# Optimization experiments

Measured on AMD Instinct MI355X. Metric: run time of the kernel, lower is better.

## Reference

```python
import jax, jax.numpy as jnp
import numpy as np

N = 100000
NNZ = 1600000
DIM = 128
IN_FEAT = 128


def spmm(vals, rows, cols, x, n):
    # sparse [n,n] COO @ dense [n,d] -> [n,d]
    return jax.ops.segment_sum(vals[:, None] * x[cols], rows, num_segments=n)


def setup_inputs() -> dict:
    key = jax.random.key(0)
    ks = jax.random.split(key, 7)
    inputs = jax.random.normal(ks[0], (N, IN_FEAT), dtype=jnp.float32)
    # TruncatedNormal(stddev=1/sqrt(fan_in)) approximated by scaled normal
    w1 = jax.random.normal(ks[1], (N, DIM), dtype=jnp.float32) / np.sqrt(N)
    w2 = jax.random.normal(ks[2], (IN_FEAT, DIM), dtype=jnp.float32) / np.sqrt(IN_FEAT)
    wg = jax.random.normal(ks[3], (DIM, 1), dtype=jnp.float32)  # glorot-ish, dim=1 gate
    A_vals = jax.random.uniform(ks[4], (NNZ,), dtype=jnp.float32)
    A_rows = jax.random.randint(ks[5], (NNZ,), 0, N, dtype=jnp.int32)
    A_cols = jax.random.randint(ks[6], (NNZ,), 0, N, dtype=jnp.int32)
    return {"inputs": inputs, "w1": w1, "w2": w2, "wg": wg,
            "A_vals": A_vals, "A_rows": A_rows, "A_cols": A_cols}


def reference(inputs, w1, w2, wg, A_vals, A_rows, A_cols):
    n = w1.shape[0]
    # aw layer: relu(A @ w1)
    a = jax.nn.relu(spmm(A_vals, A_rows, A_cols, w1, n))          # [N, dim]
    # axw layer: relu(A @ (X @ w2))
    b = jax.nn.relu(spmm(A_vals, A_rows, A_cols, inputs @ w2, n))  # [N, dim]
    # highway gate: T = sigmoid(b @ wg); y = T*a + (1-T)*b
    T = jax.nn.sigmoid(b @ wg)                                     # [N, 1]
    y = T * a + (1.0 - T) * b                                      # [N, dim]
    # final propagation: A @ y
    return spmm(A_vals, A_rows, A_cols, y, n)
```

## Files before the change

kernel.cpp:

```cpp
#include <hip/hip_runtime.h>
#include <hip/hip_bf16.h>
#include <hip/hip_fp16.h>


using f16x8 = __attribute__((ext_vector_type(8))) _Float16;
using f32x4 = __attribute__((ext_vector_type(4))) float;
using f32x2 = __attribute__((ext_vector_type(2))) float;

#define W1SCALE 128.0f
#define VSCL    3.0517578125e-05f
#define AF      (VSCL / 128.0f)
#define CHUNK   16384

__device__ __forceinline__ int block_incl_scan(int v, int* wsum) {
  int tid = threadIdx.x, lane = tid & 63, wid = tid >> 6;
  int incl = v;
#pragma unroll
  for (int off = 1; off < 64; off <<= 1) {
    int t = __shfl_up(incl, off);
    if (lane >= off) incl += t;
  }
  if (lane == 63) wsum[wid] = incl;
  __syncthreads();
  if (wid == 0) {
    int nw = (int)(blockDim.x >> 6);
    int wv = (lane < nw) ? wsum[lane] : 0;
    int wi = wv;
#pragma unroll
    for (int off = 1; off < 16; off <<= 1) {
      int t = __shfl_up(wi, off);
      if (lane >= off) wi += t;
    }
    if (lane < nw) wsum[lane] = wi - wv;
  }
  __syncthreads();
  return incl + wsum[wid];
}

__global__ __launch_bounds__(1024) void k_sortscan(const int* __restrict__ bktfill,
                                                   int* __restrict__ bktbase,
                                                   int nb, int* __restrict__ rp,
                                                   int n, int nnz) {
  __shared__ int wsum[16];
  int tid = threadIdx.x;
  int v = (tid < nb) ? bktfill[tid] : 0;
  int incl = block_incl_scan(v, wsum);
  if (tid < nb) bktbase[tid] = incl - v;
  if (tid == 0) rp[n] = nnz;
}

__global__ __launch_bounds__(1024) void k_sort3(const uint2* __restrict__ tmp,
                                                const int* __restrict__ bktfill,
                                                const int* __restrict__ bktbase,
                                                unsigned* __restrict__ ccv,
                                                int* __restrict__ rp,
                                                int n, int cap) {
  __shared__ int rcnt[256];
  __shared__ int roff[256];
  int b = blockIdx.x, tid = threadIdx.x;
  int cnt = min(bktfill[b], cap);
  const uint2* src = tmp + (size_t)b * cap;
  int bbase = bktbase[b];
  if (tid < 256) rcnt[tid] = 0;
  __syncthreads();

  unsigned rec[7];
  int rk[7], lr[7];
#pragma unroll
  for (int j = 0; j < 7; ++j) {
    int i = tid + j * 1024;
    if (i < cnt) {
      uint2 rr = src[i];
      lr[j] = (int)(rr.y & 255u);
      rec[j] = rr.x;
      rk[j] = atomicAdd(&rcnt[lr[j]], 1);
    }
  }
  __syncthreads();

  int own = (tid < 256) ? rcnt[tid] : 0;
  for (int off = 1; off < 256; off <<= 1) {
    int v = 0;
    if (tid < 256) {
      v = rcnt[tid];
      if (tid >= off) v += rcnt[tid - off];
    }
    __syncthreads();
    if (tid < 256) rcnt[tid] = v;
    __syncthreads();
  }
  if (tid < 256) {
    roff[tid] = rcnt[tid] - own;
    int row = b * 256 + tid;
    if (row < n) rp[row] = bbase + roff[tid];
  }
  __syncthreads();

#pragma unroll
  for (int j = 0; j < 7; ++j) {
    int i = tid + j * 1024;
    if (i < cnt) ccv[bbase + roff[lr[j]] + rk[j]] = rec[j];
  }
}

#define BM 256
__global__ __launch_bounds__(256) void k_gemm(const float* __restrict__ X,
                                              const float* __restrict__ w1,
                                              const float* __restrict__ W,
                                              __half* __restrict__ xw16,
                                              unsigned char* __restrict__ w1f8, int n,
                                              const int* __restrict__ Ar,
                                              const int* __restrict__ Ac,
                                              const float* __restrict__ Av,
                                              int* __restrict__ bktfill,
                                              uint2* __restrict__ tmp,
                                              int nnz, int nb, int cap, int sortB) {
  __shared__ char smem[32768];
  int tid = threadIdx.x;

  if (blockIdx.x < sortB) {
    int* hist = (int*)smem;
    int* cursor = hist + nb;
    int bi = blockIdx.x;
    int base = bi * CHUNK;
    int cnt = min(CHUNK, nnz - base);
    for (int t = tid; t < nb; t += 256) hist[t] = 0;
    __syncthreads();
    for (int it = 0; it < CHUNK / 256; ++it) {
      int k = it * 256 + tid;
      if (k < cnt) atomicAdd(&hist[Ar[base + k] >> 8], 1);
    }
    __syncthreads();
    int rot = (bi * 53) % nb;
    for (int t = tid; t < nb; t += 256) {
      int tb = t + rot;
      if (tb >= nb) tb -= nb;
      int h = hist[tb];
      int g = (h > 0) ? atomicAdd(&bktfill[tb], h) : 0;
      cursor[tb] = tb * cap + g;
    }
    __syncthreads();
    for (int it = 0; it < CHUNK / 256; ++it) {
      int k = it * 256 + tid;
      if (k < cnt) {
        int i = base + k;
        int r = Ar[i];
        int bkt = r >> 8;
        unsigned uq = (unsigned)fminf(Av[i] * 32768.f + 0.5f, 32767.f);
        int pos = atomicAdd(&cursor[bkt], 1);
        if (pos < (bkt + 1) * cap)
          tmp[pos] = make_uint2(((unsigned)Ac[i] << 15) | uq, (unsigned)r);
      }
    }
    return;
  }

  __half* lds = (__half*)smem;
  for (int t = tid; t < 2048; t += 256) {
    int nn = t >> 4, kg = t & 15;
    union { _Float16 h[8]; uint4 u; } u;
#pragma unroll
    for (int j = 0; j < 8; ++j) u.h[j] = (_Float16)W[(kg * 8 + j) * 128 + nn];
    int byte = nn * 256 + ((kg * 16) ^ ((nn & 7) << 4));
    *(uint4*)((char*)lds + byte) = u.u;
  }

  long r0 = (long)(blockIdx.x - sortB) * BM;
  for (int i = tid; i < BM * 16; i += 256) {
    int rr = i >> 4, gg = i & 15;
    long r = r0 + rr;
    if (r < n) {
      const float* src = w1 + r * 128 + gg * 8;
      float4 f0 = *(const float4*)src;
      float4 f1 = *(const float4*)(src + 4);
      int lo = __builtin_amdgcn_cvt_pk_fp8_f32(f0.x * W1SCALE, f0.y * W1SCALE, 0, false);
      lo = __builtin_amdgcn_cvt_pk_fp8_f32(f0.z * W1SCALE, f0.w * W1SCALE, lo, true);
      int hi = __builtin_amdgcn_cvt_pk_fp8_f32(f1.x * W1SCALE, f1.y * W1SCALE, 0, false);
      hi = __builtin_amdgcn_cvt_pk_fp8_f32(f1.z * W1SCALE, f1.w * W1SCALE, hi, true);
      uint2 st = {(unsigned)lo, (unsigned)hi};
      *(uint2*)(w1f8 + r * 128 + gg * 8) = st;
    }
  }
  __syncthreads();

  int wid = tid >> 6, lane = tid & 63;
  int g = lane >> 4, lm = lane & 15;
  long rowbase = r0 + wid * 64;

  f16x8 afr[4][4];
#pragma unroll
  for (int m = 0; m < 4; ++m) {
    long r = rowbase + m * 16 + lm;
    if (r >= n) r = n - 1;
    const float* xp = X + r * 128 + g * 8;
#pragma unroll
    for (int kk = 0; kk < 4; ++kk) {
      float4 lo = *(const float4*)(xp + kk * 32);
      float4 hi = *(const float4*)(xp + kk * 32 + 4);
      f16x8 a;
      a[0] = (_Float16)lo.x; a[1] = (_Float16)lo.y;
      a[2] = (_Float16)lo.z; a[3] = (_Float16)lo.w;
      a[4] = (_Float16)hi.x; a[5] = (_Float16)hi.y;
      a[6] = (_Float16)hi.z; a[7] = (_Float16)hi.w;
      afr[m][kk] = a;
    }
  }

#pragma unroll
  for (int nt = 0; nt < 8; ++nt) {
    int nn = nt * 16 + lm;
    int sw = (nn & 7) << 4;
    f16x8 bfr[4];
#pragma unroll
    for (int kk = 0; kk < 4; ++kk) {
      int byte = nn * 256 + ((kk * 64 + g * 16) ^ sw);
      bfr[kk] = *(f16x8*)((char*)lds + byte);
    }
#pragma unroll
    for (int m = 0; m < 4; ++m) {
      f32x4 acc = {0.f, 0.f, 0.f, 0.f};
#pragma unroll
      for (int kk = 0; kk < 4; ++kk)
        acc = __builtin_amdgcn_mfma_f32_16x16x32_f16(afr[m][kk], bfr[kk], acc, 0, 0, 0);
#pragma unroll
      for (int r = 0; r < 4; ++r) {
        long row = rowbase + m * 16 + g * 4 + r;
        if (row < n) xw16[row * 128 + nn] = __float2half(acc[r]);
      }
    }
  }
}

__global__ __launch_bounds__(256) void k_spmm_ab(const int* __restrict__ rp,
                                                 const unsigned* __restrict__ ccv,
                                                 const unsigned char* __restrict__ w1f8,
                                                 const __half* __restrict__ xw16,
                                                 const float* __restrict__ wg,
                                                 __half* __restrict__ y16, int n) {
  int row = (int)((blockIdx.x * 256 + threadIdx.x) >> 6);
  int lane = threadIdx.x & 63;
  if (row >= n) return;
  int s = rp[row], e = rp[row + 1];
  const unsigned char* aptr = w1f8 + lane * 2;
  const __half* bptr = xw16 + lane * 2;
  float aa0 = 0.f, aa1 = 0.f, bb0 = 0.f, bb1 = 0.f;

#define AB_EDGE(J)                                                         \
  {                                                                        \
    unsigned mm = (unsigned)__builtin_amdgcn_readlane((int)mr, (J));       \
    unsigned col = mm >> 15;                                               \
    float vq = (float)(mm & 0x7fffu);                                      \
    unsigned ua = *(const unsigned short*)(aptr + (size_t)col * 128);      \
    unsigned ub = *(const unsigned*)((const char*)bptr + (size_t)col * 256); \
    f32x2 fa = __builtin_amdgcn_cvt_pk_f32_fp8(ua, false);                 \
    float2 fb = __half22float2(*(__half2*)&ub);                            \
    aa0 = fmaf(vq, fa[0], aa0); aa1 = fmaf(vq, fa[1], aa1);                \
    bb0 = fmaf(vq, fb.x, bb0); bb1 = fmaf(vq, fb.y, bb1);                  \
  }

  for (int chunk = s; chunk < e; chunk += 64) {
    int idx = chunk + lane;
    unsigned mr = (idx < e) ? ccv[idx] : 0u;
    int cl = min(64, e - chunk);
    int j = 0;
    for (; j + 3 < cl; j += 4) {
      AB_EDGE(j) AB_EDGE(j + 1) AB_EDGE(j + 2) AB_EDGE(j + 3)
    }
    for (; j < cl; ++j) AB_EDGE(j)
  }
#undef AB_EDGE

  float a0 = fmaxf(aa0 * AF, 0.f), a1 = fmaxf(aa1 * AF, 0.f);
  float b0 = fmaxf(bb0 * VSCL, 0.f), b1 = fmaxf(bb1 * VSCL, 0.f);

  float2 wgv = *(const float2*)(wg + lane * 2);
  float part = b0 * wgv.x + b1 * wgv.y;
#pragma unroll
  for (int off = 32; off > 0; off >>= 1) part += __shfl_xor(part, off);
  float T = 1.f / (1.f + __expf(-part));
  float u = 1.f - T;

  union { __half2 h2; unsigned uu; } st;
  st.h2 = __floats2half2_rn(T * a0 + u * b0, T * a1 + u * b1);
  *(unsigned*)(y16 + (size_t)row * 128 + lane * 2) = st.uu;
}

__global__ __launch_bounds__(256) void k_spmm_out(const int* __restrict__ rp,
                                                  const unsigned* __restrict__ ccv,
                                                  const __half* __restrict__ y16,
                                                  float* __restrict__ out, int n) {
  int row = (int)((blockIdx.x * 256 + threadIdx.x) >> 6);
  int lane = threadIdx.x & 63;
  if (row >= n) return;
  int s = rp[row], e = rp[row + 1];
  const __half* ysub = y16 + lane * 2;
  float ac0 = 0.f, ac1 = 0.f;

#define OUT_EDGE(J)                                                        \
  {                                                                        \
    unsigned mm = (unsigned)__builtin_amdgcn_readlane((int)mr, (J));       \
    unsigned col = mm >> 15;                                               \
    float vq = (float)(mm & 0x7fffu);                                      \
    float2 f = __half22float2(*(const __half2*)((const char*)ysub + (size_t)col * 256)); \
    ac0 = fmaf(vq, f.x, ac0); ac1 = fmaf(vq, f.y, ac1);                    \
  }

  for (int chunk = s; chunk < e; chunk += 64) {
    int idx = chunk + lane;
    unsigned mr = (idx < e) ? ccv[idx] : 0u;
    int cl = min(64, e - chunk);
    int j = 0;
    for (; j + 3 < cl; j += 4) {
      OUT_EDGE(j) OUT_EDGE(j + 1) OUT_EDGE(j + 2) OUT_EDGE(j + 3)
    }
    for (; j < cl; ++j) OUT_EDGE(j)
  }
#undef OUT_EDGE

  union { float2 f2; long long ll; } ov;
  ov.f2.x = ac0 * VSCL;
  ov.f2.y = ac1 * VSCL;
  __builtin_nontemporal_store(ov.ll, (long long*)(out + (size_t)row * 128 + lane * 2));
}

extern "C" void kernel_launch(void* const* d_in, const int* in_sizes, int n_in,
                              void* d_out, int out_size, void* d_ws, size_t ws_size,
                              hipStream_t stream) {
  const float* X  = (const float*)d_in[0];
  const float* w1 = (const float*)d_in[1];
  const float* w2 = (const float*)d_in[2];
  const float* wg = (const float*)d_in[3];
  const float* Av = (const float*)d_in[4];
  const int*   Ar = (const int*)d_in[5];
  const int*   Ac = (const int*)d_in[6];
  float* out = (float*)d_out;
  int N   = in_sizes[0] / 128;
  int NNZ = in_sizes[4];

  int NB  = (N + 255) >> 8;
  int cap = (NNZ / NB) * 3 / 2 + 256;

  char* p = (char*)d_ws;
  auto alloc = [&](size_t b) {
    char* r = p;
    p += (b + 255) & ~(size_t)255;
    return r;
  };
  int*            rp      = (int*)alloc((size_t)(N + 1) * 4);
  int*            bktfill = (int*)alloc((size_t)NB * 4);
  int*            bktbase = (int*)alloc((size_t)NB * 4);
  uint2*          tmp     = (uint2*)alloc((size_t)NB * cap * 8);
  unsigned*       ccv     = (unsigned*)alloc((size_t)NNZ * 4);
  __half*         xw16    = (__half*)alloc((size_t)N * 128 * 2);
  unsigned char*  w1f8    = (unsigned char*)alloc((size_t)N * 128);
  __half*         y16     = (__half*)alloc((size_t)N * 128 * 2);

  hipMemsetAsync(bktfill, 0, (size_t)NB * 4, stream);

  int gemmB = (N + BM - 1) / BM;
  int sortB = (NNZ + CHUNK - 1) / CHUNK;
  k_gemm<<<sortB + gemmB, 256, 0, stream>>>(X, w1, w2, xw16, w1f8, N,
                                            Ar, Ac, Av, bktfill, tmp,
                                            NNZ, NB, cap, sortB);
  k_sortscan<<<1, 1024, 0, stream>>>(bktfill, bktbase, NB, rp, N, NNZ);
  k_sort3<<<NB, 1024, 0, stream>>>(tmp, bktfill, bktbase, ccv, rp, N, cap);
  int wb = (N + 3) / 4;
  k_spmm_ab<<<wb, 256, 0, stream>>>(rp, ccv, w1f8, xw16, wg, y16, N);
  k_spmm_out<<<wb, 256, 0, stream>>>(rp, ccv, y16, out, N);
}
```

Before: 253.4 us.

## Replace global atomic bucket reservation with per-chunk histograms and column scan

The bucket sort's first pass no longer reserves space with global atomicAdd on bktfill. Each chunk now writes its histogram to a partials matrix, a new column-scan kernel computes deterministic per-chunk offsets and bucket totals, and a separate scatter kernel places the records. CHUNK shrinks to 4096, which gives more sort blocks. This removes global atomic contention and the memset, at the cost of two extra kernel launches and rereading Ar, Ac and Av in a standalone pass that no longer overlaps with the GEMM.

```diff
diff --git a/kernel.cpp b/kernel.cpp
--- a/kernel.cpp
+++ b/kernel.cpp
@@ -10,7 +10,8 @@
 #define W1SCALE 128.0f
 #define VSCL    3.0517578125e-05f
 #define AF      (VSCL / 128.0f)
-#define CHUNK   16384
+#define CHUNK   4096
+#define MAXNB   512
 
 __device__ __forceinline__ int block_incl_scan(int v, int* wsum) {
   int tid = threadIdx.x, lane = tid & 63, wid = tid >> 6;
@@ -35,6 +36,29 @@
   }
   __syncthreads();
   return incl + wsum[wid];
+}
+
+__global__ __launch_bounds__(256) void k_colscan(const int* __restrict__ partials,
+                                                 int* __restrict__ colscanT,
+                                                 int* __restrict__ bktfill,
+                                                 int nb, int sb) {
+  int lane = threadIdx.x & 63, w = threadIdx.x >> 6;
+  int b = blockIdx.x * 4 + w;
+  if (b >= nb) return;
+  int carry = 0;
+  for (int ci0 = 0; ci0 < sb; ci0 += 64) {
+    int ci = ci0 + lane;
+    int v = (ci < sb) ? partials[(size_t)ci * nb + b] : 0;
+    int incl = v;
+#pragma unroll
+    for (int off = 1; off < 64; off <<= 1) {
+      int t = __shfl_up(incl, off);
+      if (lane >= off) incl += t;
+    }
+    if (ci < sb) colscanT[(size_t)b * sb + ci] = carry + incl - v;
+    carry += __shfl(incl, 63);
+  }
+  if (lane == 0) bktfill[b] = carry;
 }
 
 __global__ __launch_bounds__(1024) void k_sortscan(const int* __restrict__ bktfill,
@@ -47,6 +71,33 @@
   int incl = block_incl_scan(v, wsum);
   if (tid < nb) bktbase[tid] = incl - v;
   if (tid == 0) rp[n] = nnz;
+}
+
+__global__ __launch_bounds__(256) void k_scatter3(const int* __restrict__ Ar,
+                                                  const int* __restrict__ Ac,
+                                                  const float* __restrict__ Av,
+                                                  const int* __restrict__ colscanT,
+                                                  uint2* __restrict__ tmp,
+                                                  int nnz, int nb, int cap, int sb) {
+  __shared__ int cursor[MAXNB];
+  int tid = threadIdx.x, bi = blockIdx.x;
+  for (int t = tid; t < nb; t += 256)
+    cursor[t] = t * cap + colscanT[(size_t)t * sb + bi];
+  __syncthreads();
+  int base = bi * CHUNK;
+  int cnt = min(CHUNK, nnz - base);
+  for (int it = 0; it < CHUNK / 256; ++it) {
+    int k = it * 256 + tid;
+    if (k < cnt) {
+      int i = base + k;
+      int r = Ar[i];
+      int bkt = r >> 8;
+      unsigned uq = (unsigned)fminf(Av[i] * 32768.f + 0.5f, 32767.f);
+      int pos = atomicAdd(&cursor[bkt], 1);
+      if (pos < (bkt + 1) * cap)
+        tmp[pos] = make_uint2(((unsigned)Ac[i] << 15) | uq, (unsigned)r);
+    }
+  }
 }
 
 __global__ __launch_bounds__(1024) void k_sort3(const uint2* __restrict__ tmp,
@@ -110,17 +161,13 @@
                                               __half* __restrict__ xw16,
                                               unsigned char* __restrict__ w1f8, int n,
                                               const int* __restrict__ Ar,
-                                              const int* __restrict__ Ac,
-                                              const float* __restrict__ Av,
-                                              int* __restrict__ bktfill,
-                                              uint2* __restrict__ tmp,
-                                              int nnz, int nb, int cap, int sortB) {
+                                              int* __restrict__ partials,
+                                              int nnz, int nb, int sortB) {
   __shared__ char smem[32768];
   int tid = threadIdx.x;
 
   if (blockIdx.x < sortB) {
     int* hist = (int*)smem;
-    int* cursor = hist + nb;
     int bi = blockIdx.x;
     int base = bi * CHUNK;
     int cnt = min(CHUNK, nnz - base);
@@ -131,27 +178,8 @@
       if (k < cnt) atomicAdd(&hist[Ar[base + k] >> 8], 1);
     }
     __syncthreads();
-    int rot = (bi * 53) % nb;
-    for (int t = tid; t < nb; t += 256) {
-      int tb = t + rot;
-      if (tb >= nb) tb -= nb;
-      int h = hist[tb];
-      int g = (h > 0) ? atomicAdd(&bktfill[tb], h) : 0;
-      cursor[tb] = tb * cap + g;
-    }
-    __syncthreads();
-    for (int it = 0; it < CHUNK / 256; ++it) {
-      int k = it * 256 + tid;
-      if (k < cnt) {
-        int i = base + k;
-        int r = Ar[i];
-        int bkt = r >> 8;
-        unsigned uq = (unsigned)fminf(Av[i] * 32768.f + 0.5f, 32767.f);
-        int pos = atomicAdd(&cursor[bkt], 1);
-        if (pos < (bkt + 1) * cap)
-          tmp[pos] = make_uint2(((unsigned)Ac[i] << 15) | uq, (unsigned)r);
-      }
-    }
+    for (int t = tid; t < nb; t += 256)
+      partials[(size_t)bi * nb + t] = hist[t];
     return;
   }
 
@@ -337,8 +365,9 @@
   int N   = in_sizes[0] / 128;
   int NNZ = in_sizes[4];
 
-  int NB  = (N + 255) >> 8;
-  int cap = (NNZ / NB) * 3 / 2 + 256;
+  int NB    = (N + 255) >> 8;
+  int sortB = (NNZ + CHUNK - 1) / CHUNK;
+  int cap   = (NNZ / NB) * 3 / 2 + 256;
 
   char* p = (char*)d_ws;
   auto alloc = [&](size_t b) {
@@ -346,23 +375,23 @@
     p += (b + 255) & ~(size_t)255;
     return r;
   };
-  int*            rp      = (int*)alloc((size_t)(N + 1) * 4);
-  int*            bktfill = (int*)alloc((size_t)NB * 4);
-  int*            bktbase = (int*)alloc((size_t)NB * 4);
-  uint2*          tmp     = (uint2*)alloc((size_t)NB * cap * 8);
-  unsigned*       ccv     = (unsigned*)alloc((size_t)NNZ * 4);
-  __half*         xw16    = (__half*)alloc((size_t)N * 128 * 2);
-  unsigned char*  w1f8    = (unsigned char*)alloc((size_t)N * 128);
-  __half*         y16     = (__half*)alloc((size_t)N * 128 * 2);
-
-  hipMemsetAsync(bktfill, 0, (size_t)NB * 4, stream);
+  int*            rp       = (int*)alloc((size_t)(N + 1) * 4);
+  int*            partials = (int*)alloc((size_t)sortB * NB * 4);
+  int*            colscanT = (int*)alloc((size_t)NB * sortB * 4);
+  int*            bktfill  = (int*)alloc((size_t)NB * 4);
+  int*            bktbase  = (int*)alloc((size_t)NB * 4);
+  uint2*          tmp      = (uint2*)alloc((size_t)NB * cap * 8);
+  unsigned*       ccv      = (unsigned*)alloc((size_t)NNZ * 4);
+  __half*         xw16     = (__half*)alloc((size_t)N * 128 * 2);
+  unsigned char*  w1f8     = (unsigned char*)alloc((size_t)N * 128);
+  __half*         y16      = (__half*)alloc((size_t)N * 128 * 2);
 
   int gemmB = (N + BM - 1) / BM;
-  int sortB = (NNZ + CHUNK - 1) / CHUNK;
   k_gemm<<<sortB + gemmB, 256, 0, stream>>>(X, w1, w2, xw16, w1f8, N,
-                                            Ar, Ac, Av, bktfill, tmp,
-                                            NNZ, NB, cap, sortB);
+                                            Ar, partials, NNZ, NB, sortB);
+  k_colscan<<<(NB + 3) / 4, 256, 0, stream>>>(partials, colscanT, bktfill, NB, sortB);
   k_sortscan<<<1, 1024, 0, stream>>>(bktfill, bktbase, NB, rp, N, NNZ);
+  k_scatter3<<<sortB, 256, 0, stream>>>(Ar, Ac, Av, colscanT, tmp, NNZ, NB, cap, sortB);
   k_sort3<<<NB, 1024, 0, stream>>>(tmp, bktfill, bktbase, ccv, rp, N, cap);
   int wb = (N + 3) / 4;
   k_spmm_ab<<<wb, 256, 0, stream>>>(rp, ccv, w1f8, xw16, wg, y16, N);
```

After: 245.0 us. 1.03x faster.
